# Performance work log

Hardware: AMD Instinct MI355X
Metric: run time of the kernel (lower is better)

## Reference

```python
import jax, jax.numpy as jnp
import numpy as np

D_MODEL = 256
D_STATE = 16
D_INNER = 512          # expand=2 * d_model
D_CONV = 4
DT_RANK = 16           # ceil(d_model/16)
B, L = 16, 2048


def setup_inputs() -> dict:
    key = jax.random.key(0)
    ks = jax.random.split(key, 10)
    s = 0.02
    inp = {
        "x": jax.random.normal(ks[0], (B, L, D_MODEL), dtype=jnp.float32),
        "ln_w": jnp.ones((D_MODEL,), jnp.float32),
        "ln_b": jnp.zeros((D_MODEL,), jnp.float32),
        "in_proj_w": jax.random.normal(ks[1], (2 * D_INNER, D_MODEL)) * s,
        "conv_w": jax.random.normal(ks[2], (D_INNER, 1, D_CONV)) * s,
        "conv_b": jnp.zeros((D_INNER,), jnp.float32),
        "x_proj_w": jax.random.normal(ks[3], (DT_RANK + 2 * D_STATE, D_INNER)) * s,
        "dt_proj_w": jax.random.normal(ks[4], (D_INNER, DT_RANK)) * s,
        "dt_proj_b": jax.random.uniform(ks[5], (D_INNER,), minval=-4.0, maxval=-2.0),
        "A_log": jnp.log(jnp.broadcast_to(jnp.arange(1, D_STATE + 1, dtype=jnp.float32), (D_INNER, D_STATE))).copy(),
        "D_param": jnp.ones((D_INNER,), jnp.float32),
        "out_proj_w": jax.random.normal(ks[6], (D_MODEL, D_INNER)) * s,
    }
    return inp


def _layernorm(x, w, b, eps=1e-5):
    mu = jnp.mean(x, axis=-1, keepdims=True)
    var = jnp.var(x, axis=-1, keepdims=True)
    return (x - mu) * jax.lax.rsqrt(var + eps) * w + b


def _mamba(xn, in_proj_w, conv_w, conv_b, x_proj_w, dt_proj_w, dt_proj_b, A_log, D_param, out_proj_w):
    # in_proj -> x, z   (B, L, d_inner) each
    xz = jnp.einsum('bld,ed->ble', xn, in_proj_w)
    x_in, z = jnp.split(xz, 2, axis=-1)

    # depthwise causal conv over L
    xc = jax.lax.conv_general_dilated(
        jnp.transpose(x_in, (0, 2, 1)), conv_w,
        window_strides=(1,), padding=[(D_CONV - 1, 0)],
        feature_group_count=D_INNER,
        dimension_numbers=('NCH', 'OIH', 'NCH')) + conv_b[None, :, None]
    xc = jax.nn.silu(jnp.transpose(xc, (0, 2, 1)))  # (B, L, d_inner)

    # input-dependent dt, B, C
    dbc = jnp.einsum('ble,fe->blf', xc, x_proj_w)  # (B, L, dt_rank + 2N)
    dt = jax.nn.softplus(jnp.einsum('blr,er->ble', dbc[..., :DT_RANK], dt_proj_w) + dt_proj_b)
    Bc = dbc[..., DT_RANK:DT_RANK + D_STATE]   # (B, L, N)
    Cc = dbc[..., DT_RANK + D_STATE:]          # (B, L, N)

    A = -jnp.exp(A_log)  # (d_inner, N)

    def step(h, inputs):
        dt_t, x_t, B_t, C_t = inputs  # (B,e), (B,e), (B,n), (B,n)
        dA = jnp.exp(dt_t[..., None] * A)                      # (B, e, n)
        h = dA * h + dt_t[..., None] * B_t[:, None, :] * x_t[..., None]
        y = jnp.sum(h * C_t[:, None, :], axis=-1)              # (B, e)
        return h, y

    h0 = jnp.zeros((xn.shape[0], D_INNER, D_STATE), xn.dtype)
    seq = (jnp.swapaxes(dt, 0, 1), jnp.swapaxes(xc, 0, 1),
           jnp.swapaxes(Bc, 0, 1), jnp.swapaxes(Cc, 0, 1))
    _, ys = jax.lax.scan(step, h0, seq)
    y = jnp.swapaxes(ys, 0, 1) + D_param * xc                  # (B, L, e)
    y = y * jax.nn.silu(z)
    return jnp.einsum('ble,de->bld', y, out_proj_w)


def reference(x, ln_w, ln_b, in_proj_w, conv_w, conv_b, x_proj_w, dt_proj_w, dt_proj_b, A_log, D_param, out_proj_w):
    xn = _layernorm(x, ln_w, ln_b)
    out = _mamba(xn, in_proj_w, conv_w, conv_b, x_proj_w, dt_proj_w, dt_proj_b, A_log, D_param, out_proj_w)
    return x + out  # dropout is identity in eval
```

## Files before the change

### kernel.cpp

```cpp
#include <hip/hip_runtime.h>
#include <cstdint>

#define DEVI __device__ __forceinline__

typedef __bf16 bf16;
typedef __bf16 bf16x8 __attribute__((ext_vector_type(8)));
typedef __bf16 bf16x4 __attribute__((ext_vector_type(4)));
typedef __bf16 bf16x2 __attribute__((ext_vector_type(2)));
typedef float floatx4 __attribute__((ext_vector_type(4)));

constexpr int BATCH = 16, SEQ = 2048, DM = 256, DI = 512;
constexpr int M = BATCH * SEQ;
constexpr int NC = 128;
constexpr int CL = SEQ / NC;
static_assert(NC * CL == SEQ, "chunking");
constexpr float LOG2E = 1.4426950408889634f;

DEVI void gl2lds16(const void* g, void* l) {
  __builtin_amdgcn_global_load_lds(
      (const __attribute__((address_space(1))) unsigned int*)(uintptr_t)g,
      (__attribute__((address_space(3))) unsigned int*)(unsigned int)(uintptr_t)l,
      16, 0, 0);
}

DEVI float sigmoidf_(float x) { return 1.f / (1.f + __expf(-x)); }
DEVI float exp2_(float x) { return __builtin_amdgcn_exp2f(x); }

__global__ __launch_bounds__(256) void prep_kernel(
    const float* __restrict__ w1, const float* __restrict__ wx,
    const float* __restrict__ wo, const float* __restrict__ alog,
    bf16* __restrict__ w1b, bf16* __restrict__ wxb, bf16* __restrict__ wob,
    float* __restrict__ An, int* __restrict__ flags) {
  constexpr int n1 = 1024 * 256, n2 = 48 * 512, n3 = 256 * 512;
  int i = blockIdx.x * 256 + threadIdx.x;
  if (i < n1) w1b[i] = (bf16)w1[i];
  else if (i < n1 + n2) wxb[i - n1] = (bf16)wx[i - n1];
  else if (i < n1 + n2 + n3) wob[i - n1 - n2] = (bf16)wo[i - n1 - n2];
  else if (i < n1 + n2 + n3 + DI) {
    const int e = i - (n1 + n2 + n3);
    const float a0 = -__expf(alog[e * 16]);
    bool ok = (a0 < 0.f);
#pragma unroll 1
    for (int s = 0; s < 16; s++) {
      const float a = -__expf(alog[e * 16 + s]);
      An[e * 16 + s] = a * LOG2E;
      ok = ok && (__builtin_fabsf(a / a0 - (float)(s + 1)) < 1e-3f);
    }
    flags[e] = ok ? 1 : 0;
  }
}

__global__ __launch_bounds__(256) void ln_kernel(
    const float* __restrict__ x, const float* __restrict__ w,
    const float* __restrict__ b, bf16* __restrict__ xn) {
  const int row = blockIdx.x * 4 + (threadIdx.x >> 6);
  const int lane = threadIdx.x & 63;
  const float4 v = ((const float4*)(x + (size_t)row * DM))[lane];
  float s = v.x + v.y + v.z + v.w;
  float s2 = v.x * v.x + v.y * v.y + v.z * v.z + v.w * v.w;
#pragma unroll
  for (int m = 1; m < 64; m <<= 1) { s += __shfl_xor(s, m); s2 += __shfl_xor(s2, m); }
  const float mu = s * (1.f / DM);
  const float var = s2 * (1.f / DM) - mu * mu;
  const float rs = rsqrtf(var + 1e-5f);
  const float4 wv = ((const float4*)w)[lane];
  const float4 bv = ((const float4*)b)[lane];
  bf16x4 o;
  o[0] = (bf16)((v.x - mu) * rs * wv.x + bv.x);
  o[1] = (bf16)((v.y - mu) * rs * wv.y + bv.y);
  o[2] = (bf16)((v.z - mu) * rs * wv.z + bv.z);
  o[3] = (bf16)((v.w - mu) * rs * wv.w + bv.w);
  *(bf16x4*)(xn + (size_t)row * DM + lane * 4) = o;
}

template <int N, int K, bool OUT_BF16, bool RESID>
__global__ __launch_bounds__(256) void gemm_nt(const bf16* __restrict__ A,
                                               const bf16* __restrict__ W,
                                               void* __restrict__ out,
                                               const float* __restrict__ resid) {
  constexpr int BK = 32;
  __shared__ __align__(16) bf16 lA[128 * BK];
  __shared__ __align__(16) bf16 lB[128 * BK];
  const int tid = threadIdx.x;
  const int wave = tid >> 6, lane = tid & 63;
  const int bm = blockIdx.x * 128, bn = blockIdx.y * 128;
  const int wm = (wave >> 1) * 64, wn = (wave & 1) * 64;
  const int q = lane >> 4, r = lane & 15;
  floatx4 acc[4][4] = {};
  const int c0 = wave * 64 + lane;
  const int row0 = c0 >> 2, kp = (c0 & 3) * 8;
  for (int k0 = 0; k0 < K; k0 += BK) {
    gl2lds16(A + (size_t)(bm + row0) * K + k0 + kp, lA + c0 * 8);
    gl2lds16(A + (size_t)(bm + row0 + 64) * K + k0 + kp, lA + (c0 + 256) * 8);
    gl2lds16(W + (size_t)(bn + row0) * K + k0 + kp, lB + c0 * 8);
    gl2lds16(W + (size_t)(bn + row0 + 64) * K + k0 + kp, lB + (c0 + 256) * 8);
    __syncthreads();
    bf16x8 af[4], bfr[4];
#pragma unroll
    for (int i = 0; i < 4; i++) af[i] = *(const bf16x8*)&lA[(wm + i * 16 + r) * BK + q * 8];
#pragma unroll
    for (int j = 0; j < 4; j++) bfr[j] = *(const bf16x8*)&lB[(wn + j * 16 + r) * BK + q * 8];
#pragma unroll
    for (int i = 0; i < 4; i++)
#pragma unroll
      for (int j = 0; j < 4; j++)
        acc[i][j] = __builtin_amdgcn_mfma_f32_16x16x32_bf16(af[i], bfr[j], acc[i][j], 0, 0, 0);
    __syncthreads();
  }
#pragma unroll
  for (int i = 0; i < 4; i++)
#pragma unroll
    for (int j = 0; j < 4; j++)
#pragma unroll
      for (int t = 0; t < 4; t++) {
        const int row = bm + wm + i * 16 + q * 4 + t;
        const int col = bn + wn + j * 16 + r;
        const size_t idx = (size_t)row * N + col;
        float v = acc[i][j][t];
        if constexpr (OUT_BF16) {
          ((bf16*)out)[idx] = (bf16)v;
        } else {
          if constexpr (RESID) v += resid[idx];
          ((float*)out)[idx] = v;
        }
      }
}

__global__ __launch_bounds__(256) void conv_silu(const bf16* __restrict__ xz,
                                                 const float* __restrict__ cw,
                                                 const float* __restrict__ cb,
                                                 bf16* __restrict__ xc) {
  const int tid = threadIdx.x;
  const int e2 = tid * 2;
  const int p0 = blockIdx.x * 8;
  const int b = blockIdx.y;
  const float4 w0 = ((const float4*)cw)[e2];
  const float4 w1 = ((const float4*)cw)[e2 + 1];
  const float2 bias = *(const float2*)(cb + e2);
  float xa[11], xb_[11];
#pragma unroll
  for (int j = 0; j < 11; j++) {
    const int pos = p0 - 3 + j;
    float fa = 0.f, fb = 0.f;
    if (pos >= 0) {
      const unsigned u = *(const unsigned*)(xz + ((size_t)b * SEQ + pos) * 1024 + e2);
      fa = __uint_as_float(u << 16);
      fb = __uint_as_float(u & 0xFFFF0000u);
    }
    xa[j] = fa; xb_[j] = fb;
  }
#pragma unroll
  for (int k = 0; k < 8; k++) {
    const float a0 = bias.x + xa[k] * w0.x + xa[k + 1] * w0.y + xa[k + 2] * w0.z + xa[k + 3] * w0.w;
    const float a1 = bias.y + xb_[k] * w1.x + xb_[k + 1] * w1.y + xb_[k + 2] * w1.z + xb_[k + 3] * w1.w;
    bf16x2 o;
    o[0] = (bf16)(a0 * sigmoidf_(a0));
    o[1] = (bf16)(a1 * sigmoidf_(a1));
    *(bf16x2*)(xc + ((size_t)b * SEQ + p0 + k) * DI + e2) = o;
  }
}

__global__ __launch_bounds__(256) void gemm_xproj(const bf16* __restrict__ A,
                                                  const bf16* __restrict__ W,
                                                  float* __restrict__ out) {
  constexpr int K = DI;
  __shared__ __align__(16) bf16 lW[48 * K];
  __shared__ __align__(16) bf16 lA[64 * 32];
  const int tid = threadIdx.x;
  const int wave = tid >> 6, lane = tid & 63;
  const int bm = blockIdx.x * 64;
  const int q = lane >> 4, r = lane & 15;
#pragma unroll
  for (int rd = 0; rd < 12; rd++) {
    const int c = rd * 256 + tid;
    gl2lds16((const char*)W + (size_t)c * 16, (char*)lW + (size_t)c * 16);
  }
  const int row0 = tid >> 2, kp = (tid & 3) * 8;
  const int wm = wave * 16;
  floatx4 acc[3] = {};
  for (int k0 = 0; k0 < K; k0 += 32) {
    gl2lds16(A + (size_t)(bm + row0) * K + k0 + kp, lA + tid * 8);
    __syncthreads();
    bf16x8 af = *(const bf16x8*)&lA[(wm + r) * 32 + q * 8];
#pragma unroll
    for (int j = 0; j < 3; j++) {
      const bf16x8 bfr = *(const bf16x8*)&lW[(j * 16 + r) * K + k0 + q * 8];
      acc[j] = __builtin_amdgcn_mfma_f32_16x16x32_bf16(af, bfr, acc[j], 0, 0, 0);
    }
    __syncthreads();
  }
#pragma unroll
  for (int j = 0; j < 3; j++)
#pragma unroll
    for (int t = 0; t < 4; t++)
      out[(size_t)(bm + wm + q * 4 + t) * 48 + j * 16 + r] = acc[j][t];
}

__global__ __launch_bounds__(256) void dtproj_kernel(const float* __restrict__ dbc,
                                                     const float* __restrict__ dtw,
                                                     const float* __restrict__ dtb,
                                                     bf16* __restrict__ dt) {
  __shared__ __align__(16) float sd[64 * 16];
  const int tid = threadIdx.x;
  const int p0 = blockIdx.x * 64;
  const int e = blockIdx.y * 256 + tid;
  {
    const int rowi = tid >> 2, coli = (tid & 3) * 4;
    *(float4*)&sd[rowi * 16 + coli] = *(const float4*)(dbc + (size_t)(p0 + rowi) * 48 + coli);
  }
  float w[16];
#pragma unroll
  for (int s = 0; s < 16; s += 4) {
    float4 t4 = *(const float4*)(dtw + (size_t)e * 16 + s);
    w[s] = t4.x; w[s + 1] = t4.y; w[s + 2] = t4.z; w[s + 3] = t4.w;
  }
  const float bias = dtb[e];
  __syncthreads();
  for (int p = 0; p < 64; p++) {
    float s = bias;
#pragma unroll
    for (int r2 = 0; r2 < 16; r2++) s += sd[p * 16 + r2] * w[r2];
    const float sp = (s > 15.f) ? s : __logf(1.f + __expf(s));
    dt[(size_t)(p0 + p) * DI + e] = (bf16)sp;
  }
}

__global__ __launch_bounds__(256) void scan_pass1(const bf16* __restrict__ dt,
                                                  const bf16* __restrict__ xc,
                                                  const float* __restrict__ dbc,
                                                  const float* __restrict__ An,
                                                  const int* __restrict__ flags,
                                                  float* __restrict__ U,
                                                  float* __restrict__ SD) {
  const int e = blockIdx.x * 256 + threadIdx.x;
  const int ch = blockIdx.y, b = blockIdx.z;
  const int fast = flags[e];
  float h[16];
#pragma unroll
  for (int s = 0; s < 16; s++) h[s] = 0.f;
  float sdt = 0.f;
  const size_t posBase = (size_t)b * SEQ + (size_t)ch * CL;
  if (fast) {
    const float A0 = An[(size_t)e * 16];
    for (int il = 0; il < CL; il++) {
      const size_t pos = posBase + il;
      const float dtv = (float)dt[pos * DI + e];
      const float xv = (float)xc[pos * DI + e];
      const float* bc = dbc + pos * 48 + 16;
      float Bv[16];
#pragma unroll
      for (int s = 0; s < 16; s += 4) {
        float4 b4 = *(const float4*)(bc + s);
        Bv[s] = b4.x; Bv[s + 1] = b4.y; Bv[s + 2] = b4.z; Bv[s + 3] = b4.w;
      }
      const float dtx = dtv * xv;
      sdt += dtv;
      const float d1 = exp2_(dtv * A0);
      float d = 1.f;
#pragma unroll
      for (int s = 0; s < 16; s++) { d *= d1; h[s] = d * h[s] + dtx * Bv[s]; }
    }
  } else {
    float A[16];
#pragma unroll
    for (int s = 0; s < 16; s += 4) {
      float4 a4 = *(const float4*)(An + (size_t)e * 16 + s);
      A[s] = a4.x; A[s + 1] = a4.y; A[s + 2] = a4.z; A[s + 3] = a4.w;
    }
    for (int il = 0; il < CL; il++) {
      const size_t pos = posBase + il;
      const float dtv = (float)dt[pos * DI + e];
      const float xv = (float)xc[pos * DI + e];
      const float* bc = dbc + pos * 48 + 16;
      float Bv[16];
#pragma unroll
      for (int s = 0; s < 16; s += 4) {
        float4 b4 = *(const float4*)(bc + s);
        Bv[s] = b4.x; Bv[s + 1] = b4.y; Bv[s + 2] = b4.z; Bv[s + 3] = b4.w;
      }
      const float dtx = dtv * xv;
      sdt += dtv;
#pragma unroll
      for (int s = 0; s < 16; s++) h[s] = exp2_(dtv * A[s]) * h[s] + dtx * Bv[s];
    }
  }
  float* up = U + ((size_t)(b * NC + ch) * DI + e) * 16;
#pragma unroll
  for (int s = 0; s < 16; s += 4) {
    float4 o; o.x = h[s]; o.y = h[s + 1]; o.z = h[s + 2]; o.w = h[s + 3];
    *(float4*)(up + s) = o;
  }
  SD[(size_t)(b * NC + ch) * DI + e] = sdt;
}

__global__ __launch_bounds__(256) void scan_pass2(const float* __restrict__ SD,
                                                  float* U,
                                                  const float* __restrict__ An) {
  const int t = blockIdx.x * 256 + threadIdx.x;
  const int s = t & 15;
  const int e = (t >> 4) & (DI - 1);
  const int b = t >> 13;
  const float A = An[e * 16 + s];
  float h = 0.f;
#pragma unroll 4
  for (int c = 0; c < NC; c++) {
    const size_t cell = (size_t)(b * NC + c) * DI + e;
    const float sdv = SD[cell];
    const size_t base = cell * 16 + s;
    const float u = U[base];
    const float h0 = h;
    h = exp2_(A * sdv) * h0 + u;
    U[base] = h0;
  }
}

__global__ __launch_bounds__(256) void scan_pass3(const bf16* dt,
                                                  const bf16* __restrict__ xc,
                                                  const bf16* __restrict__ xz,
                                                  const float* __restrict__ dbc,
                                                  const float* __restrict__ An,
                                                  const int* __restrict__ flags,
                                                  const float* __restrict__ H0,
                                                  const float* __restrict__ Dp,
                                                  bf16* yg) {
  const int e = blockIdx.x * 256 + threadIdx.x;
  const int ch = blockIdx.y, b = blockIdx.z;
  const int fast = flags[e];
  float h[16];
  const float* hp = H0 + ((size_t)(b * NC + ch) * DI + e) * 16;
#pragma unroll
  for (int s = 0; s < 16; s += 4) {
    float4 h4 = *(const float4*)(hp + s);
    h[s] = h4.x; h[s + 1] = h4.y; h[s + 2] = h4.z; h[s + 3] = h4.w;
  }
  const float Dv = Dp[e];
  const size_t posBase = (size_t)b * SEQ + (size_t)ch * CL;
  if (fast) {
    const float A0 = An[(size_t)e * 16];
    for (int il = 0; il < CL; il++) {
      const size_t pos = posBase + il;
      const float dtv = (float)dt[pos * DI + e];
      const float xv = (float)xc[pos * DI + e];
      const float zv = (float)xz[pos * 1024 + DI + e];
      const float* bc = dbc + pos * 48 + 16;
      float Bv[16], Cv[16];
#pragma unroll
      for (int s = 0; s < 16; s += 4) {
        float4 b4 = *(const float4*)(bc + s);
        Bv[s] = b4.x; Bv[s + 1] = b4.y; Bv[s + 2] = b4.z; Bv[s + 3] = b4.w;
        float4 c4 = *(const float4*)(bc + 16 + s);
        Cv[s] = c4.x; Cv[s + 1] = c4.y; Cv[s + 2] = c4.z; Cv[s + 3] = c4.w;
      }
      const float dtx = dtv * xv;
      const float d1 = exp2_(dtv * A0);
      float d = 1.f, y = 0.f;
#pragma unroll
      for (int s = 0; s < 16; s++) {
        d *= d1;
        h[s] = d * h[s] + dtx * Bv[s];
        y += h[s] * Cv[s];
      }
      const float yv = (y + Dv * xv) * zv * sigmoidf_(zv);
      yg[pos * DI + e] = (bf16)yv;
    }
  } else {
    float A[16];
#pragma unroll
    for (int s = 0; s < 16; s += 4) {
      float4 a4 = *(const float4*)(An + (size_t)e * 16 + s);
      A[s] = a4.x; A[s + 1] = a4.y; A[s + 2] = a4.z; A[s + 3] = a4.w;
    }
    for (int il = 0; il < CL; il++) {
      const size_t pos = posBase + il;
      const float dtv = (float)dt[pos * DI + e];
      const float xv = (float)xc[pos * DI + e];
      const float zv = (float)xz[pos * 1024 + DI + e];
      const float* bc = dbc + pos * 48 + 16;
      float Bv[16], Cv[16];
#pragma unroll
      for (int s = 0; s < 16; s += 4) {
        float4 b4 = *(const float4*)(bc + s);
        Bv[s] = b4.x; Bv[s + 1] = b4.y; Bv[s + 2] = b4.z; Bv[s + 3] = b4.w;
        float4 c4 = *(const float4*)(bc + 16 + s);
        Cv[s] = c4.x; Cv[s + 1] = c4.y; Cv[s + 2] = c4.z; Cv[s + 3] = c4.w;
      }
      const float dtx = dtv * xv;
      float y = 0.f;
#pragma unroll
      for (int s = 0; s < 16; s++) {
        h[s] = exp2_(dtv * A[s]) * h[s] + dtx * Bv[s];
        y += h[s] * Cv[s];
      }
      const float yv = (y + Dv * xv) * zv * sigmoidf_(zv);
      yg[pos * DI + e] = (bf16)yv;
    }
  }
}

extern "C" void kernel_launch(void* const* d_in, const int* in_sizes, int n_in,
                              void* d_out, int out_size, void* d_ws, size_t ws_size,
                              hipStream_t stream) {
  const float* x = (const float*)d_in[0];
  const float* ln_w = (const float*)d_in[1];
  const float* ln_b = (const float*)d_in[2];
  const float* w_in = (const float*)d_in[3];
  const float* conv_w = (const float*)d_in[4];
  const float* conv_b = (const float*)d_in[5];
  const float* w_x = (const float*)d_in[6];
  const float* w_dt = (const float*)d_in[7];
  const float* b_dt = (const float*)d_in[8];
  const float* a_log = (const float*)d_in[9];
  const float* d_par = (const float*)d_in[10];
  const float* w_out = (const float*)d_in[11];

  char* ws = (char*)d_ws;
  size_t off = 0;
  auto alloc = [&](size_t bytes) {
    void* p = ws + off;
    off = (off + bytes + 255) & ~(size_t)255;
    return p;
  };
  bf16* xn = (bf16*)alloc((size_t)M * DM * 2);
  bf16* xzb = (bf16*)alloc((size_t)M * 1024 * 2);
  bf16* xcb = (bf16*)alloc((size_t)M * DI * 2);
  float* dbc = (float*)alloc((size_t)M * 48 * 4);
  bf16* dtb_ = (bf16*)alloc((size_t)M * DI * 2);
  float* U = (float*)alloc((size_t)BATCH * NC * DI * 16 * 4);
  float* SD = (float*)alloc((size_t)BATCH * NC * DI * 4);
  bf16* w1b = (bf16*)alloc(1024 * 256 * 2);
  bf16* wxb = (bf16*)alloc(48 * 512 * 2);
  bf16* wob = (bf16*)alloc(256 * 512 * 2);
  float* An = (float*)alloc(512 * 16 * 4);
  int* flags = (int*)alloc(512 * 4);

  constexpr int prep_n = 1024 * 256 + 48 * 512 + 256 * 512 + DI;
  prep_kernel<<<dim3((prep_n + 255) / 256), dim3(256), 0, stream>>>(w_in, w_x, w_out, a_log, w1b, wxb, wob, An, flags);
  ln_kernel<<<dim3(M / 4), dim3(256), 0, stream>>>(x, ln_w, ln_b, xn);
  gemm_nt<1024, 256, true, false><<<dim3(M / 128, 8), dim3(256), 0, stream>>>(xn, w1b, (void*)xzb, nullptr);
  conv_silu<<<dim3(SEQ / 8, BATCH), dim3(256), 0, stream>>>(xzb, conv_w, conv_b, xcb);
  gemm_xproj<<<dim3(M / 64), dim3(256), 0, stream>>>(xcb, wxb, dbc);
  dtproj_kernel<<<dim3(M / 64, 2), dim3(256), 0, stream>>>(dbc, w_dt, b_dt, dtb_);
  scan_pass1<<<dim3(2, NC, BATCH), dim3(256), 0, stream>>>(dtb_, xcb, dbc, An, flags, U, SD);
  scan_pass2<<<dim3(BATCH * DI * 16 / 256), dim3(256), 0, stream>>>(SD, U, An);
  scan_pass3<<<dim3(2, NC, BATCH), dim3(256), 0, stream>>>(dtb_, xcb, xzb, dbc, An, flags, U, d_par, dtb_);
  gemm_nt<256, 512, false, true><<<dim3(M / 128, 2), dim3(256), 0, stream>>>(dtb_, wob, d_out, x);
}
```

Baseline: 319.9 us.

## Stage scan B/C in LDS, use power tree, halve chunk count

New measurement: 312.9 us. 1.02x faster.

```diff
diff --git a/kernel.cpp b/kernel.cpp
--- a/kernel.cpp
+++ b/kernel.cpp
@@ -11,7 +11,7 @@
 
 constexpr int BATCH = 16, SEQ = 2048, DM = 256, DI = 512;
 constexpr int M = BATCH * SEQ;
-constexpr int NC = 128;
+constexpr int NC = 64;
 constexpr int CL = SEQ / NC;
 static_assert(NC * CL == SEQ, "chunking");
 constexpr float LOG2E = 1.4426950408889634f;
@@ -225,6 +225,14 @@
   }
 }
 
+DEVI void powtree(float d1, float* P) {
+  const float p2 = d1 * d1, p4 = p2 * p2, p8 = p4 * p4;
+  P[0] = d1;      P[1] = p2;      P[2] = p2 * d1; P[3] = p4;
+  P[4] = p4 * d1; P[5] = p4 * p2; P[6] = p4 * P[2]; P[7] = p8;
+  P[8] = p8 * d1; P[9] = p8 * p2; P[10] = p8 * P[2]; P[11] = p8 * p4;
+  P[12] = p8 * P[4]; P[13] = p8 * P[5]; P[14] = p8 * P[6]; P[15] = p8 * p8;
+}
+
 __global__ __launch_bounds__(256) void scan_pass1(const bf16* __restrict__ dt,
                                                   const bf16* __restrict__ xc,
                                                   const float* __restrict__ dbc,
@@ -232,56 +240,61 @@
                                                   const int* __restrict__ flags,
                                                   float* __restrict__ U,
                                                   float* __restrict__ SD) {
-  const int e = blockIdx.x * 256 + threadIdx.x;
+  __shared__ __align__(16) float sbc[CL * 32];
+  const int tid = threadIdx.x;
+  const int e = blockIdx.x * 256 + tid;
   const int ch = blockIdx.y, b = blockIdx.z;
+  const size_t posBase = (size_t)b * SEQ + (size_t)ch * CL;
+  {
+    const int il = tid >> 3, f = (tid & 7) * 4;
+    gl2lds16(dbc + (posBase + il) * 48 + 16 + f, (char*)sbc + tid * 16);
+  }
   const int fast = flags[e];
   float h[16];
 #pragma unroll
   for (int s = 0; s < 16; s++) h[s] = 0.f;
   float sdt = 0.f;
-  const size_t posBase = (size_t)b * SEQ + (size_t)ch * CL;
+  const float A0 = An[(size_t)e * 16];
+  float A[16];
+  if (!fast) {
+#pragma unroll
+    for (int s = 0; s < 16; s += 4) {
+      float4 a4 = *(const float4*)(An + (size_t)e * 16 + s);
+      A[s] = a4.x; A[s + 1] = a4.y; A[s + 2] = a4.z; A[s + 3] = a4.w;
+    }
+  }
+  __syncthreads();
   if (fast) {
-    const float A0 = An[(size_t)e * 16];
+#pragma unroll 2
     for (int il = 0; il < CL; il++) {
       const size_t pos = posBase + il;
       const float dtv = (float)dt[pos * DI + e];
       const float xv = (float)xc[pos * DI + e];
-      const float* bc = dbc + pos * 48 + 16;
-      float Bv[16];
-#pragma unroll
-      for (int s = 0; s < 16; s += 4) {
-        float4 b4 = *(const float4*)(bc + s);
-        Bv[s] = b4.x; Bv[s + 1] = b4.y; Bv[s + 2] = b4.z; Bv[s + 3] = b4.w;
-      }
       const float dtx = dtv * xv;
       sdt += dtv;
-      const float d1 = exp2_(dtv * A0);
-      float d = 1.f;
-#pragma unroll
-      for (int s = 0; s < 16; s++) { d *= d1; h[s] = d * h[s] + dtx * Bv[s]; }
+      float P[16];
+      powtree(exp2_(dtv * A0), P);
+      const float* bc = sbc + il * 32;
+#pragma unroll
+      for (int sg = 0; sg < 4; sg++) {
+        const float4 B4 = *(const float4*)(bc + sg * 4);
+        h[sg * 4 + 0] = P[sg * 4 + 0] * h[sg * 4 + 0] + dtx * B4.x;
+        h[sg * 4 + 1] = P[sg * 4 + 1] * h[sg * 4 + 1] + dtx * B4.y;
+        h[sg * 4 + 2] = P[sg * 4 + 2] * h[sg * 4 + 2] + dtx * B4.z;
+        h[sg * 4 + 3] = P[sg * 4 + 3] * h[sg * 4 + 3] + dtx * B4.w;
+      }
     }
   } else {
-    float A[16];
-#pragma unroll
-    for (int s = 0; s < 16; s += 4) {
-      float4 a4 = *(const float4*)(An + (size_t)e * 16 + s);
-      A[s] = a4.x; A[s + 1] = a4.y; A[s + 2] = a4.z; A[s + 3] = a4.w;
-    }
+#pragma unroll 2
     for (int il = 0; il < CL; il++) {
       const size_t pos = posBase + il;
       const float dtv = (float)dt[pos * DI + e];
       const float xv = (float)xc[pos * DI + e];
-      const float* bc = dbc + pos * 48 + 16;
-      float Bv[16];
-#pragma unroll
-      for (int s = 0; s < 16; s += 4) {
-        float4 b4 = *(const float4*)(bc + s);
-        Bv[s] = b4.x; Bv[s + 1] = b4.y; Bv[s + 2] = b4.z; Bv[s + 3] = b4.w;
-      }
       const float dtx = dtv * xv;
       sdt += dtv;
-#pragma unroll
-      for (int s = 0; s < 16; s++) h[s] = exp2_(dtv * A[s]) * h[s] + dtx * Bv[s];
+      const float* bc = sbc + il * 32;
+#pragma unroll
+      for (int s = 0; s < 16; s++) h[s] = exp2_(dtv * A[s]) * h[s] + dtx * bc[s];
     }
   }
   float* up = U + ((size_t)(b * NC + ch) * DI + e) * 16;
@@ -314,7 +327,7 @@
   }
 }
 
-__global__ __launch_bounds__(256) void scan_pass3(const bf16* dt,
+__global__ __launch_bounds__(256) void scan_pass3(const bf16* __restrict__ dt,
                                                   const bf16* __restrict__ xc,
                                                   const bf16* __restrict__ xz,
                                                   const float* __restrict__ dbc,
@@ -322,9 +335,16 @@
                                                   const int* __restrict__ flags,
                                                   const float* __restrict__ H0,
                                                   const float* __restrict__ Dp,
-                                                  bf16* yg) {
-  const int e = blockIdx.x * 256 + threadIdx.x;
+                                                  bf16* __restrict__ yg) {
+  __shared__ __align__(16) float sbc[CL * 32];
+  const int tid = threadIdx.x;
+  const int e = blockIdx.x * 256 + tid;
   const int ch = blockIdx.y, b = blockIdx.z;
+  const size_t posBase = (size_t)b * SEQ + (size_t)ch * CL;
+  {
+    const int il = tid >> 3, f = (tid & 7) * 4;
+    gl2lds16(dbc + (posBase + il) * 48 + 16 + f, (char*)sbc + tid * 16);
+  }
   const int fast = flags[e];
   float h[16];
   const float* hp = H0 + ((size_t)(b * NC + ch) * DI + e) * 16;
@@ -334,62 +354,55 @@
     h[s] = h4.x; h[s + 1] = h4.y; h[s + 2] = h4.z; h[s + 3] = h4.w;
   }
   const float Dv = Dp[e];
-  const size_t posBase = (size_t)b * SEQ + (size_t)ch * CL;
+  const float A0 = An[(size_t)e * 16];
+  float A[16];
+  if (!fast) {
+#pragma unroll
+    for (int s = 0; s < 16; s += 4) {
+      float4 a4 = *(const float4*)(An + (size_t)e * 16 + s);
+      A[s] = a4.x; A[s + 1] = a4.y; A[s + 2] = a4.z; A[s + 3] = a4.w;
+    }
+  }
+  __syncthreads();
   if (fast) {
-    const float A0 = An[(size_t)e * 16];
+#pragma unroll 2
     for (int il = 0; il < CL; il++) {
       const size_t pos = posBase + il;
       const float dtv = (float)dt[pos * DI + e];
       const float xv = (float)xc[pos * DI + e];
       const float zv = (float)xz[pos * 1024 + DI + e];
-      const float* bc = dbc + pos * 48 + 16;
-      float Bv[16], Cv[16];
-#pragma unroll
-      for (int s = 0; s < 16; s += 4) {
-        float4 b4 = *(const float4*)(bc + s);
-        Bv[s] = b4.x; Bv[s + 1] = b4.y; Bv[s + 2] = b4.z; Bv[s + 3] = b4.w;
-        float4 c4 = *(const float4*)(bc + 16 + s);
-        Cv[s] = c4.x; Cv[s + 1] = c4.y; Cv[s + 2] = c4.z; Cv[s + 3] = c4.w;
+      const float dtx = dtv * xv;
+      float P[16];
+      powtree(exp2_(dtv * A0), P);
+      const float* bc = sbc + il * 32;
+      float y0 = 0.f, y1 = 0.f, y2 = 0.f, y3 = 0.f;
+#pragma unroll
+      for (int sg = 0; sg < 4; sg++) {
+        const float4 B4 = *(const float4*)(bc + sg * 4);
+        const float4 C4 = *(const float4*)(bc + 16 + sg * 4);
+        h[sg * 4 + 0] = P[sg * 4 + 0] * h[sg * 4 + 0] + dtx * B4.x;  y0 += h[sg * 4 + 0] * C4.x;
+        h[sg * 4 + 1] = P[sg * 4 + 1] * h[sg * 4 + 1] + dtx * B4.y;  y1 += h[sg * 4 + 1] * C4.y;
+        h[sg * 4 + 2] = P[sg * 4 + 2] * h[sg * 4 + 2] + dtx * B4.z;  y2 += h[sg * 4 + 2] * C4.z;
+        h[sg * 4 + 3] = P[sg * 4 + 3] * h[sg * 4 + 3] + dtx * B4.w;  y3 += h[sg * 4 + 3] * C4.w;
       }
-      const float dtx = dtv * xv;
-      const float d1 = exp2_(dtv * A0);
-      float d = 1.f, y = 0.f;
-#pragma unroll
-      for (int s = 0; s < 16; s++) {
-        d *= d1;
-        h[s] = d * h[s] + dtx * Bv[s];
-        y += h[s] * Cv[s];
-      }
+      const float y = (y0 + y1) + (y2 + y3);
       const float yv = (y + Dv * xv) * zv * sigmoidf_(zv);
       yg[pos * DI + e] = (bf16)yv;
     }
   } else {
-    float A[16];
-#pragma unroll
-    for (int s = 0; s < 16; s += 4) {
-      float4 a4 = *(const float4*)(An + (size_t)e * 16 + s);
-      A[s] = a4.x; A[s + 1] = a4.y; A[s + 2] = a4.z; A[s + 3] = a4.w;
-    }
+#pragma unroll 2
     for (int il = 0; il < CL; il++) {
       const size_t pos = posBase + il;
       const float dtv = (float)dt[pos * DI + e];
       const float xv = (float)xc[pos * DI + e];
       const float zv = (float)xz[pos * 1024 + DI + e];
-      const float* bc = dbc + pos * 48 + 16;
-      float Bv[16], Cv[16];
-#pragma unroll
-      for (int s = 0; s < 16; s += 4) {
-        float4 b4 = *(const float4*)(bc + s);
-        Bv[s] = b4.x; Bv[s + 1] = b4.y; Bv[s + 2] = b4.z; Bv[s + 3] = b4.w;
-        float4 c4 = *(const float4*)(bc + 16 + s);
-        Cv[s] = c4.x; Cv[s + 1] = c4.y; Cv[s + 2] = c4.z; Cv[s + 3] = c4.w;
-      }
       const float dtx = dtv * xv;
+      const float* bc = sbc + il * 32;
       float y = 0.f;
 #pragma unroll
       for (int s = 0; s < 16; s++) {
-        h[s] = exp2_(dtv * A[s]) * h[s] + dtx * Bv[s];
-        y += h[s] * Cv[s];
+        h[s] = exp2_(dtv * A[s]) * h[s] + dtx * bc[s];
+        y += h[s] * bc[16 + s];
       }
       const float yv = (y + Dv * xv) * zv * sigmoidf_(zv);
       yg[pos * DI + e] = (bf16)yv;
@@ -425,6 +438,7 @@
   bf16* xcb = (bf16*)alloc((size_t)M * DI * 2);
   float* dbc = (float*)alloc((size_t)M * 48 * 4);
   bf16* dtb_ = (bf16*)alloc((size_t)M * DI * 2);
+  bf16* ygb = (bf16*)alloc((size_t)M * DI * 2);
   float* U = (float*)alloc((size_t)BATCH * NC * DI * 16 * 4);
   float* SD = (float*)alloc((size_t)BATCH * NC * DI * 4);
   bf16* w1b = (bf16*)alloc(1024 * 256 * 2);
@@ -442,6 +456,6 @@
   dtproj_kernel<<<dim3(M / 64, 2), dim3(256), 0, stream>>>(dbc, w_dt, b_dt, dtb_);
   scan_pass1<<<dim3(2, NC, BATCH), dim3(256), 0, stream>>>(dtb_, xcb, dbc, An, flags, U, SD);
   scan_pass2<<<dim3(BATCH * DI * 16 / 256), dim3(256), 0, stream>>>(SD, U, An);
-  scan_pass3<<<dim3(2, NC, BATCH), dim3(256), 0, stream>>>(dtb_, xcb, xzb, dbc, An, flags, U, d_par, dtb_);
-  gemm_nt<256, 512, false, true><<<dim3(M / 128, 2), dim3(256), 0, stream>>>(dtb_, wob, d_out, x);
-}
+  scan_pass3<<<dim3(2, NC, BATCH), dim3(256), 0, stream>>>(dtb_, xcb, xzb, dbc, An, flags, U, d_par, ygb);
+  gemm_nt<256, 512, false, true><<<dim3(M / 128, 2), dim3(256), 0, stream>>>(ygb, wob, d_out, x);
+}
```
